# Optimization experiments

Measured on AMD Instinct MI355X. Metric: run time of the kernel, lower is better.

Reference implementation:

```python
import jax, jax.numpy as jnp
import numpy as np

B, S, E, H = 8, 2048, 512, 8
D = E // H  # head_dim = 64


def setup_inputs() -> dict:
    key0 = jax.random.key(0)
    ks = jax.random.split(key0, 12)
    scale = 1.0 / np.sqrt(E)
    return {
        "value": jax.random.normal(ks[0], (B, S, E), jnp.float32),
        "key": jax.random.normal(ks[1], (B, S, E), jnp.float32),
        "query": jax.random.normal(ks[2], (B, S, E), jnp.float32),
        "mask": jax.random.randint(ks[3], (B, 1, 1, S), 0, 2, jnp.int32),
        "wq": jax.random.normal(ks[4], (E, E), jnp.float32) * scale,
        "bq": jnp.zeros((E,), jnp.float32),
        "wk": jax.random.normal(ks[5], (E, E), jnp.float32) * scale,
        "bk": jnp.zeros((E,), jnp.float32),
        "wv": jax.random.normal(ks[6], (E, E), jnp.float32) * scale,
        "bv": jnp.zeros((E,), jnp.float32),
        "wo": jax.random.normal(ks[7], (E, E), jnp.float32) * scale,
        "bo": jnp.zeros((E,), jnp.float32),
    }


def reference(value, key, query, mask, wq, bq, wk, bk, wv, bv, wo, bo):
    b, s, e = query.shape
    # projections
    q = (query @ wq + bq).reshape(b, s, H, D)  # (B,S,H,D)
    k = (key @ wk + bk).reshape(b, s, H, D)
    v = (value @ wv + bv).reshape(b, s, H, D)
    # scaled dot-product logits: (B,H,Sq,Sk)
    logits = jnp.einsum("bqhd,bkhd->bhqk", q, k) / jnp.sqrt(jnp.asarray(D, q.dtype))
    logits = logits + mask.astype(logits.dtype) * -1e9  # mask==1 -> blocked
    attn = jax.nn.softmax(logits, axis=-1)
    out = jnp.einsum("bhqk,bkhd->bqhd", attn, v).reshape(b, s, e)
    return out @ wo + bo
```

## Files before the change

kernel.cpp:

```cpp
#include <hip/hip_runtime.h>

#define Bz 8
#define Sz 2048
#define Ez 512
#define Hz 8
#define Dz 64

typedef _Float16 f16;
typedef __attribute__((ext_vector_type(2))) _Float16 f16x2;
typedef __attribute__((ext_vector_type(8))) _Float16 f16x8;
typedef __attribute__((ext_vector_type(4))) float f32x4;

#define LOG2E 1.44269504f

__device__ __forceinline__ void async16(const void* g, void* l) {
    __builtin_amdgcn_global_load_lds(
        (const __attribute__((address_space(1))) unsigned int*)g,
        (__attribute__((address_space(3))) unsigned int*)l, 16, 0, 0);
}

__device__ __forceinline__ f16x2 pkrtz(float a, float b) {
    return __builtin_bit_cast(f16x2, __builtin_amdgcn_cvt_pkrtz(a, b));
}

__device__ __forceinline__ int swz(int row) {
    return (row & 7) ^ ((2 * ((row >> 3) & 3)) & 7);
}

__global__ __launch_bounds__(256)
void cast_kernel(const float* __restrict__ q, const float* __restrict__ k,
                 const float* __restrict__ v, const int* __restrict__ mask,
                 f16* __restrict__ qa, f16* __restrict__ ka, f16* __restrict__ va,
                 int* __restrict__ idx, int* __restrict__ slen)
{
    const int z = blockIdx.y;
    const int tid = threadIdx.x;
    if (z == 3) {
        const int b = blockIdx.x;
        if (b >= Bz) return;
        __shared__ int sc2[2][256];
        __shared__ int stot;
        const int* mp = mask + (size_t)b * Sz;
        int m[8], c = 0;
        #pragma unroll
        for (int j = 0; j < 8; ++j) { m[j] = mp[tid*8 + j]; c += (m[j] == 0); }
        sc2[0][tid] = c;
        __syncthreads();
        int src = 0;
        #pragma unroll
        for (int s = 1; s < 256; s <<= 1) {
            int vv = sc2[src][tid] + ((tid >= s) ? sc2[src][tid - s] : 0);
            sc2[src ^ 1][tid] = vv;
            src ^= 1;
            __syncthreads();
        }
        int incl = sc2[src][tid];
        int base = incl - c;
        if (tid == 255) { slen[b] = incl; stot = incl; }
        int kk = base;
        #pragma unroll
        for (int j = 0; j < 8; ++j)
            if (m[j] == 0) idx[(size_t)b * Sz + (kk++)] = tid*8 + j;
        __syncthreads();
        for (int j = stot + tid; j < Sz; j += 256) idx[(size_t)b * Sz + j] = 0;
        return;
    }
    const int i = blockIdx.x * 256 + tid;
    const float* src = (z == 0) ? q : (z == 1) ? k : v;
    f16* dst = (z == 0) ? qa : (z == 1) ? ka : va;
    float4 x = *(const float4*)&src[(size_t)i * 4];
    f16x2 h0 = pkrtz(x.x, x.y), h1 = pkrtz(x.z, x.w);
    f16 h[4] = {h0[0], h0[1], h1[0], h1[1]};
    *(uint2*)&dst[(size_t)i * 4] = *(uint2*)h;
}

__global__ __launch_bounds__(256)
void prep_w(const float* __restrict__ W0, const float* __restrict__ W1,
            const float* __restrict__ W2, const float* __restrict__ W3,
            f16* __restrict__ T0, f16* __restrict__ T1,
            f16* __restrict__ T2, f16* __restrict__ T3)
{
    __shared__ float S[64][68];
    const float* W = (blockIdx.z==0)?W0:(blockIdx.z==1)?W1:(blockIdx.z==2)?W2:W3;
    f16*         T = (blockIdx.z==0)?T0:(blockIdx.z==1)?T1:(blockIdx.z==2)?T2:T3;
    const float sc = (blockIdx.z == 0) ? 0.125f * LOG2E : 1.0f;
    const int k0 = blockIdx.x * 64, n0 = blockIdx.y * 64;
    const int tid = threadIdx.x;
    {
        int kr = tid >> 4, nc = (tid & 15) * 4;
        #pragma unroll
        for (int i = 0; i < 4; ++i) {
            float4 w4 = *(const float4*)&W[(size_t)(k0 + kr + i*16) * Ez + n0 + nc];
            S[kr + i*16][nc+0] = w4.x; S[kr + i*16][nc+1] = w4.y;
            S[kr + i*16][nc+2] = w4.z; S[kr + i*16][nc+3] = w4.w;
        }
    }
    __syncthreads();
    {
        int n = tid >> 2, kq = tid & 3;
        f16 h[16];
        #pragma unroll
        for (int j = 0; j < 16; ++j) h[j] = (f16)(S[kq*16 + j][n] * sc);
        f16* dst = &T[(size_t)(n0 + n) * Ez + k0 + kq*16];
        *(uint4*)&dst[0] = *(uint4*)&h[0];
        *(uint4*)&dst[8] = *(uint4*)&h[8];
    }
}

__global__ __launch_bounds__(256)
void compact_v(const f16* __restrict__ vp, const int* __restrict__ idx,
               const int* __restrict__ slen, f16* __restrict__ vt)
{
    const int ct = blockIdx.x, h = blockIdx.y, b = blockIdx.z;
    const int sl = slen[b];
    if (ct * 64 >= sl && !(ct == 0 && sl == 0)) return;
    __shared__ f16 S[64 * 72];
    const int tid = threadIdx.x;
    {
        int r = tid >> 2, ch = tid & 3;
        int j = ct * 64 + r;
        uint4 v0 = {0,0,0,0}, v1 = {0,0,0,0};
        if (j < sl) {
            int s = idx[(size_t)b * Sz + j];
            const f16* srcp = vp + (((size_t)b * Hz + h) * Sz + s) * Dz + ch * 16;
            v0 = *(const uint4*)&srcp[0];
            v1 = *(const uint4*)&srcp[8];
        }
        *(uint4*)&S[r*72 + ch*16]     = v0;
        *(uint4*)&S[r*72 + ch*16 + 8] = v1;
    }
    __syncthreads();
    {
        int d = tid >> 2, kq = tid & 3;
        f16 hh[16];
        #pragma unroll
        for (int j = 0; j < 16; ++j) hh[j] = S[(kq*16 + j)*72 + d];
        f16* dst = vt + (((size_t)b * Hz + h) * Dz + d) * Sz + ct*64 + kq*16;
        *(uint4*)&dst[0] = *(uint4*)&hh[0];
        *(uint4*)&dst[8] = *(uint4*)&hh[8];
    }
}

__global__ __launch_bounds__(256, 4)
void proj_gemm(const f16* __restrict__ qa, const f16* __restrict__ ka,
               const f16* __restrict__ va,
               const f16* __restrict__ wtq, const f16* __restrict__ wtk,
               const f16* __restrict__ wtv,
               const float* __restrict__ bqp, const float* __restrict__ bkp,
               const float* __restrict__ bvp,
               f16* __restrict__ qp, f16* __restrict__ kp, f16* __restrict__ vp)
{
    __shared__ __align__(16) char lds[32768];
    const int z = blockIdx.z;
    const f16* A  = (z==0)?qa:(z==1)?ka:va;
    const f16* Wt = (z==0)?wtq:(z==1)?wtk:wtv;
    const float* bias = (z==0)?bqp:(z==1)?bkp:bvp;
    f16* C16 = (z==0)?qp:(z==1)?kp:vp;
    const float bscale = (z==0) ? 0.125f*LOG2E : 1.0f;

    const int tid  = threadIdx.x;
    const int lane = tid & 63, w = tid >> 6;
    const int col  = lane & 15, quad = lane >> 4;
    const int wm = w & 1, wn = w >> 1;
    const int m0 = blockIdx.x * 128, n0 = blockIdx.y * 128;
    const int srow = lane >> 2, schunk = lane & 3;

    f32x4 acc[4][4];
    #pragma unroll
    for (int i = 0; i < 4; ++i)
        #pragma unroll
        for (int j = 0; j < 4; ++j) acc[i][j] = (f32x4){0.f,0.f,0.f,0.f};

    auto issue = [&](int t, int buf) {
        f16* As = (f16*)(lds + buf * 16384);
        f16* Ws = As + 4096;
        #pragma unroll
        for (int i = 0; i < 2; ++i) {
            int row = w*32 + i*16 + srow;
            int cl = schunk ^ ((row >> 1) & 3);
            async16(&A[(size_t)(m0 + row) * Ez + t*32 + cl*8],  &As[row*32 + schunk*8]);
            async16(&Wt[(size_t)(n0 + row) * Ez + t*32 + cl*8], &Ws[row*32 + schunk*8]);
        }
    };

    issue(0, 0);
    const int xrc = (col >> 1) & 3;

    for (int t = 0; t < 16; ++t) {
        const int cur = t & 1;
        __syncthreads();
        if (t < 15) issue(t + 1, cur ^ 1);
        f16* As = (f16*)(lds + cur * 16384);
        f16* Ws = As + 4096;
        f16x8 af[4];
        #pragma unroll
        for (int mi = 0; mi < 4; ++mi)
            af[mi] = *(const f16x8*)&As[(wm*64 + mi*16 + col)*32 + ((quad ^ xrc)*8)];
        #pragma unroll
        for (int ni = 0; ni < 4; ++ni) {
            f16x8 wf = *(const f16x8*)&Ws[(wn*64 + ni*16 + col)*32 + ((quad ^ xrc)*8)];
            #pragma unroll
            for (int mi = 0; mi < 4; ++mi)
                acc[mi][ni] = __builtin_amdgcn_mfma_f32_16x16x32_f16(af[mi], wf, acc[mi][ni], 0,0,0);
        }
    }

    f16* Tr = (f16*)lds;
    #pragma unroll
    for (int p = 0; p < 2; ++p) {
        __syncthreads();
        if (wn == p) {
            #pragma unroll
            for (int ni = 0; ni < 4; ++ni) {
                float bv = bias[n0 + p*64 + ni*16 + col] * bscale;
                #pragma unroll
                for (int mi = 0; mi < 4; ++mi)
                    #pragma unroll
                    for (int rr = 0; rr < 4; ++rr) {
                        int ml = wm*64 + mi*16 + quad*4 + rr;
                        Tr[ml*72 + ni*16 + col] = (f16)(acc[mi][ni][rr] + bv);
                    }
            }
        }
        __syncthreads();
        int rw = tid >> 1, half = tid & 1;
        int m = m0 + rw, b = m >> 11, s = m & (Sz-1);
        int hh = (n0 >> 6) + p;
        f16* dst = &C16[(((size_t)b*Hz + hh)*Sz + s)*Dz + half*32];
        const f16* srcp = &Tr[rw*72 + half*32];
        #pragma unroll
        for (int j = 0; j < 4; ++j)
            *(uint4*)&dst[j*8] = *(const uint4*)&srcp[j*8];
    }
}

__global__ __launch_bounds__(256, 4)
void out_gemm(const f16* __restrict__ A, const f16* __restrict__ Wt,
              const float* __restrict__ bias, float* __restrict__ Cf)
{
    __shared__ __align__(16) char lds[32768];
    const int tid  = threadIdx.x;
    const int lane = tid & 63, w = tid >> 6;
    const int col  = lane & 15, quad = lane >> 4;
    const int wm = w & 1, wn = w >> 1;
    const int m0 = blockIdx.x * 128, n0 = blockIdx.y * 128;
    const int srow = lane >> 2, schunk = lane & 3;

    f32x4 acc[4][4];
    #pragma unroll
    for (int i = 0; i < 4; ++i)
        #pragma unroll
        for (int j = 0; j < 4; ++j) acc[i][j] = (f32x4){0.f,0.f,0.f,0.f};

    auto issue = [&](int t, int buf) {
        f16* As = (f16*)(lds + buf * 16384);
        f16* Ws = As + 4096;
        #pragma unroll
        for (int i = 0; i < 2; ++i) {
            int row = w*32 + i*16 + srow;
            int cl = schunk ^ ((row >> 1) & 3);
            async16(&A[(size_t)(m0 + row) * Ez + t*32 + cl*8],  &As[row*32 + schunk*8]);
            async16(&Wt[(size_t)(n0 + row) * Ez + t*32 + cl*8], &Ws[row*32 + schunk*8]);
        }
    };

    issue(0, 0);
    const int xrc = (col >> 1) & 3;

    for (int t = 0; t < 16; ++t) {
        const int cur = t & 1;
        __syncthreads();
        if (t < 15) issue(t + 1, cur ^ 1);
        f16* As = (f16*)(lds + cur * 16384);
        f16* Ws = As + 4096;
        f16x8 af[4];
        #pragma unroll
        for (int mi = 0; mi < 4; ++mi)
            af[mi] = *(const f16x8*)&As[(wm*64 + mi*16 + col)*32 + ((quad ^ xrc)*8)];
        #pragma unroll
        for (int ni = 0; ni < 4; ++ni) {
            f16x8 wf = *(const f16x8*)&Ws[(wn*64 + ni*16 + col)*32 + ((quad ^ xrc)*8)];
            #pragma unroll
            for (int mi = 0; mi < 4; ++mi)
                acc[mi][ni] = __builtin_amdgcn_mfma_f32_16x16x32_f16(af[mi], wf, acc[mi][ni], 0,0,0);
        }
    }

    #pragma unroll
    for (int ni = 0; ni < 4; ++ni) {
        int n = n0 + wn*64 + ni*16 + col;
        float bv = bias[n];
        #pragma unroll
        for (int mi = 0; mi < 4; ++mi)
            #pragma unroll
            for (int rr = 0; rr < 4; ++rr) {
                int m = m0 + wm*64 + mi*16 + quad*4 + rr;
                Cf[(size_t)m * Ez + n] = acc[mi][ni][rr] + bv;
            }
    }
}

__global__ __launch_bounds__(256, 4)
void attn_f16(const f16* __restrict__ Q, const f16* __restrict__ K,
              const f16* __restrict__ VT, const int* __restrict__ idx,
              const int* __restrict__ slen, f16* __restrict__ O)
{
    __shared__ __align__(16) f16 KS[2][64*64];
    __shared__ __align__(16) f16 VS[2][64*64];

    const int tid  = threadIdx.x;
    const int lane = tid & 63, w = tid >> 6;
    const int col  = lane & 15, quad = lane >> 4;

    const int blk = blockIdx.x;
    const int xcd = blk & 7, slot = blk >> 3;
    const int bh = xcd + 8 * (slot >> 4);
    const int qb = slot & 15;
    const int b = bh >> 3, h = bh & 7;

    const int sl = slen[b];
    int nt = (sl + 63) >> 6;
    if (nt < 1) nt = 1;

    const int q0 = qb * 128 + w * 32;

    f16x8 qf[2][2];
    #pragma unroll
    for (int qt = 0; qt < 2; ++qt)
        #pragma unroll
        for (int ks = 0; ks < 2; ++ks)
            qf[qt][ks] = *(const f16x8*)&Q[((size_t)bh*Sz + q0 + qt*16 + col)*Dz + ks*32 + quad*8];

    const f16* Kp = K + (size_t)bh * Sz * Dz;
    const f16* Vp = VT + (size_t)bh * Dz * Sz;
    const int* ixp = idx + (size_t)b * Sz;

    const int srow = lane >> 3, sch = lane & 7;
    const int row0 = w*16 + srow, row1 = row0 + 8;
    const int cl0 = sch ^ swz(row0), cl1 = sch ^ swz(row1);

    int keyrow[4], gk[4];
    #pragma unroll
    for (int kc = 0; kc < 4; ++kc) {
        keyrow[kc] = 32*(kc>>1) + 8*(col>>2) + 4*(kc&1) + (col&3);
        gk[kc] = swz(keyrow[kc]);
    }

    f32x4 oacc[2][4];
    #pragma unroll
    for (int qt = 0; qt < 2; ++qt)
        #pragma unroll
        for (int dc = 0; dc < 4; ++dc) oacc[qt][dc] = (f32x4){0.f,0.f,0.f,0.f};
    const f32x4 zero4 = (f32x4){0.f, 0.f, 0.f, 0.f};
    f32x4 lacc[2] = {(f32x4){0.f,0.f,0.f,0.f}, (f32x4){0.f,0.f,0.f,0.f}};
    f16x8 one8;
    #pragma unroll
    for (int i = 0; i < 8; ++i) one8[i] = (f16)1.0f;

    auto issue = [&](int t, int buf, int s0, int s1) {
        async16(&Kp[(size_t)s0*Dz + cl0*8],          &KS[buf][row0*64 + sch*8]);
        async16(&Vp[(size_t)row0*Sz + t*64 + cl0*8], &VS[buf][row0*64 + sch*8]);
        async16(&Kp[(size_t)s1*Dz + cl1*8],          &KS[buf][row1*64 + sch*8]);
        async16(&Vp[(size_t)row1*Sz + t*64 + cl1*8], &VS[buf][row1*64 + sch*8]);
    };

    int cs0 = ixp[row0], cs1 = ixp[row1];
    issue(0, 0, cs0, cs1);
    int ns0 = 0, ns1 = 0;
    if (nt > 1) { ns0 = ixp[64 + row0]; ns1 = ixp[64 + row1]; }

    for (int t = 0; t < nt; ++t) {
        const int cur = t & 1;
        __syncthreads();
        if (t + 1 < nt) {
            issue(t + 1, cur ^ 1, ns0, ns1);
            if (t + 2 < nt) {
                ns0 = ixp[(t+2)*64 + row0];
                ns1 = ixp[(t+2)*64 + row1];
            }
        }

        f32x4 sc[2][4];
        __builtin_amdgcn_s_setprio(1);
        #pragma unroll
        for (int kc = 0; kc < 4; ++kc) {
            f16x8 kf0 = *(const f16x8*)&KS[cur][keyrow[kc]*64 + ((quad ^ gk[kc])*8)];
            f16x8 kf1 = *(const f16x8*)&KS[cur][keyrow[kc]*64 + (((4 + quad) ^ gk[kc])*8)];
            sc[0][kc] = __builtin_amdgcn_mfma_f32_16x16x32_f16(kf0, qf[0][0], zero4, 0,0,0);
            sc[1][kc] = __builtin_amdgcn_mfma_f32_16x16x32_f16(kf0, qf[1][0], zero4, 0,0,0);
            sc[0][kc] = __builtin_amdgcn_mfma_f32_16x16x32_f16(kf1, qf[0][1], sc[0][kc], 0,0,0);
            sc[1][kc] = __builtin_amdgcn_mfma_f32_16x16x32_f16(kf1, qf[1][1], sc[1][kc], 0,0,0);
        }
        __builtin_amdgcn_s_setprio(0);

        const bool last = (t == nt - 1);
        union { f16x2 h2[4]; f16x8 h8; } ph[2][2];
        #pragma unroll
        for (int qt = 0; qt < 2; ++qt) {
            #pragma unroll
            for (int kg = 0; kg < 2; ++kg) {
                float e0 = __builtin_amdgcn_exp2f(sc[qt][2*kg][0]);
                float e1 = __builtin_amdgcn_exp2f(sc[qt][2*kg][1]);
                float e2 = __builtin_amdgcn_exp2f(sc[qt][2*kg][2]);
                float e3 = __builtin_amdgcn_exp2f(sc[qt][2*kg][3]);
                float e4 = __builtin_amdgcn_exp2f(sc[qt][2*kg+1][0]);
                float e5 = __builtin_amdgcn_exp2f(sc[qt][2*kg+1][1]);
                float e6 = __builtin_amdgcn_exp2f(sc[qt][2*kg+1][2]);
                float e7 = __builtin_amdgcn_exp2f(sc[qt][2*kg+1][3]);
                if (last) {
                    int rem = sl - t*64 - 32*kg - 8*quad;
                    e0 = (rem > 0) ? e0 : 0.f; e1 = (rem > 1) ? e1 : 0.f;
                    e2 = (rem > 2) ? e2 : 0.f; e3 = (rem > 3) ? e3 : 0.f;
                    e4 = (rem > 4) ? e4 : 0.f; e5 = (rem > 5) ? e5 : 0.f;
                    e6 = (rem > 6) ? e6 : 0.f; e7 = (rem > 7) ? e7 : 0.f;
                }
                ph[qt][kg].h2[0] = pkrtz(e0, e1);
                ph[qt][kg].h2[1] = pkrtz(e2, e3);
                ph[qt][kg].h2[2] = pkrtz(e4, e5);
                ph[qt][kg].h2[3] = pkrtz(e6, e7);
            }
        }

        __builtin_amdgcn_s_setprio(1);
        lacc[0] = __builtin_amdgcn_mfma_f32_16x16x32_f16(one8, ph[0][0].h8, lacc[0], 0,0,0);
        lacc[1] = __builtin_amdgcn_mfma_f32_16x16x32_f16(one8, ph[1][0].h8, lacc[1], 0,0,0);
        lacc[0] = __builtin_amdgcn_mfma_f32_16x16x32_f16(one8, ph[0][1].h8, lacc[0], 0,0,0);
        lacc[1] = __builtin_amdgcn_mfma_f32_16x16x32_f16(one8, ph[1][1].h8, lacc[1], 0,0,0);
        #pragma unroll
        for (int dc = 0; dc < 4; ++dc) {
            const int d = dc*16 + col;
            const int gd = swz(d);
            #pragma unroll
            for (int kg = 0; kg < 2; ++kg) {
                f16x8 vf = *(const f16x8*)&VS[cur][d*64 + (((kg*4 + quad) ^ gd)*8)];
                oacc[0][dc] = __builtin_amdgcn_mfma_f32_16x16x32_f16(vf, ph[0][kg].h8, oacc[0][dc], 0,0,0);
                oacc[1][dc] = __builtin_amdgcn_mfma_f32_16x16x32_f16(vf, ph[1][kg].h8, oacc[1][dc], 0,0,0);
            }
        }
        __builtin_amdgcn_s_setprio(0);
    }

    float inv[2];
    inv[0] = 1.0f / lacc[0][0];
    inv[1] = 1.0f / lacc[1][0];
    #pragma unroll
    for (int qt = 0; qt < 2; ++qt) {
        const int q = q0 + qt*16 + col;
        f16* op = &O[((size_t)b*Sz + q)*Ez + h*Dz];
        #pragma unroll
        for (int dc = 0; dc < 4; ++dc) {
            f16 ov[4] = {(f16)(oacc[qt][dc][0]*inv[qt]), (f16)(oacc[qt][dc][1]*inv[qt]),
                         (f16)(oacc[qt][dc][2]*inv[qt]), (f16)(oacc[qt][dc][3]*inv[qt])};
            *(uint2*)&op[dc*16 + quad*4] = *(uint2*)ov;
        }
    }
}

extern "C" void kernel_launch(void* const* d_in, const int* in_sizes, int n_in,
                              void* d_out, int out_size, void* d_ws, size_t ws_size,
                              hipStream_t stream)
{
    const float* value = (const float*)d_in[0];
    const float* key   = (const float*)d_in[1];
    const float* query = (const float*)d_in[2];
    const int*   mask  = (const int*)d_in[3];
    const float* wq = (const float*)d_in[4];
    const float* bq = (const float*)d_in[5];
    const float* wk = (const float*)d_in[6];
    const float* bk = (const float*)d_in[7];
    const float* wv = (const float*)d_in[8];
    const float* bv = (const float*)d_in[9];
    const float* wo = (const float*)d_in[10];
    const float* bo = (const float*)d_in[11];
    float* out = (float*)d_out;

    const size_t nW   = (size_t)Ez * Ez;
    const size_t nAct = (size_t)Bz * Sz * Ez;
    f16* wtq = (f16*)d_ws;
    f16* wtk = wtq + nW;
    f16* wtv = wtk + nW;
    f16* wto = wtv + nW;
    f16* qa  = wto + nW;
    f16* ka  = qa + nAct;
    f16* va  = ka + nAct;
    f16* qp  = va + nAct;
    f16* kp  = qp + nAct;
    f16* vp  = kp + nAct;
    f16* vt  = vp + nAct;
    f16* o16 = vt + nAct;
    int* idxp = (int*)(o16 + nAct);
    int* slenp = idxp + Bz * Sz;

    cast_kernel<<<dim3(8192, 4), 256, 0, stream>>>(query, key, value, mask,
                                                   qa, ka, va, idxp, slenp);
    prep_w<<<dim3(8, 8, 4), 256, 0, stream>>>(wq, wk, wv, wo, wtq, wtk, wtv, wto);

    proj_gemm<<<dim3(128, 4, 3), 256, 0, stream>>>(qa, ka, va, wtq, wtk, wtv,
                                                   bq, bk, bv, qp, kp, vp);

    compact_v<<<dim3(32, Hz, Bz), 256, 0, stream>>>(vp, idxp, slenp, vt);

    attn_f16<<<1024, 256, 0, stream>>>(qp, kp, vt, idxp, slenp, o16);

    out_gemm<<<dim3(128, 4), 256, 0, stream>>>(o16, wto, bo, out);
}
```

Measured before the change: 281.4 us.

## Scatter K/V into compacted order in projection epilogue instead of gathering in attention

The mask prefix-scan now emits a per-position rank (or -1 for masked keys) instead of a list of gather indices. The K/V projection epilogue uses this rank to write unmasked rows directly to compacted positions and skips storing masked rows. As a result, compact_v and the attention kernel read contiguous rows, with no index lookups and no dependent index loads in the async prefetch loop. The trade-off is that rows past the compacted length in K are no longer padded with valid data, so correctness relies on the last-tile masking in attention.

```diff
diff --git a/kernel.cpp b/kernel.cpp
--- a/kernel.cpp
+++ b/kernel.cpp
@@ -31,7 +31,7 @@
 void cast_kernel(const float* __restrict__ q, const float* __restrict__ k,
                  const float* __restrict__ v, const int* __restrict__ mask,
                  f16* __restrict__ qa, f16* __restrict__ ka, f16* __restrict__ va,
-                 int* __restrict__ idx, int* __restrict__ slen)
+                 int* __restrict__ rnk, int* __restrict__ slen)
 {
     const int z = blockIdx.y;
     const int tid = threadIdx.x;
@@ -39,7 +39,6 @@
         const int b = blockIdx.x;
         if (b >= Bz) return;
         __shared__ int sc2[2][256];
-        __shared__ int stot;
         const int* mp = mask + (size_t)b * Sz;
         int m[8], c = 0;
         #pragma unroll
@@ -56,13 +55,16 @@
         }
         int incl = sc2[src][tid];
         int base = incl - c;
-        if (tid == 255) { slen[b] = incl; stot = incl; }
+        if (tid == 255) slen[b] = incl;
         int kk = base;
-        #pragma unroll
-        for (int j = 0; j < 8; ++j)
-            if (m[j] == 0) idx[(size_t)b * Sz + (kk++)] = tid*8 + j;
-        __syncthreads();
-        for (int j = stot + tid; j < Sz; j += 256) idx[(size_t)b * Sz + j] = 0;
+        int r8[8];
+        #pragma unroll
+        for (int j = 0; j < 8; ++j) {
+            r8[j] = (m[j] == 0) ? kk : -1;
+            kk += (m[j] == 0);
+        }
+        #pragma unroll
+        for (int j = 0; j < 8; ++j) rnk[(size_t)b * Sz + tid*8 + j] = r8[j];
         return;
     }
     const int i = blockIdx.x * 256 + tid;
@@ -108,8 +110,8 @@
 }
 
 __global__ __launch_bounds__(256)
-void compact_v(const f16* __restrict__ vp, const int* __restrict__ idx,
-               const int* __restrict__ slen, f16* __restrict__ vt)
+void compact_v(const f16* __restrict__ vp, const int* __restrict__ slen,
+               f16* __restrict__ vt)
 {
     const int ct = blockIdx.x, h = blockIdx.y, b = blockIdx.z;
     const int sl = slen[b];
@@ -121,8 +123,7 @@
         int j = ct * 64 + r;
         uint4 v0 = {0,0,0,0}, v1 = {0,0,0,0};
         if (j < sl) {
-            int s = idx[(size_t)b * Sz + j];
-            const f16* srcp = vp + (((size_t)b * Hz + h) * Sz + s) * Dz + ch * 16;
+            const f16* srcp = vp + (((size_t)b * Hz + h) * Sz + j) * Dz + ch * 16;
             v0 = *(const uint4*)&srcp[0];
             v1 = *(const uint4*)&srcp[8];
         }
@@ -147,7 +148,7 @@
                const f16* __restrict__ wtq, const f16* __restrict__ wtk,
                const f16* __restrict__ wtv,
                const float* __restrict__ bqp, const float* __restrict__ bkp,
-               const float* __restrict__ bvp,
+               const float* __restrict__ bvp, const int* __restrict__ rnk,
                f16* __restrict__ qp, f16* __restrict__ kp, f16* __restrict__ vp)
 {
     __shared__ __align__(16) char lds[32768];
@@ -203,6 +204,16 @@
             for (int mi = 0; mi < 4; ++mi)
                 acc[mi][ni] = __builtin_amdgcn_mfma_f32_16x16x32_f16(af[mi], wf, acc[mi][ni], 0,0,0);
         }
+    }
+
+    const int rw = tid >> 1, half = tid & 1;
+    const int m = m0 + rw, b = m >> 11, s = m & (Sz-1);
+    int rowout = s;
+    bool dostore = true;
+    if (z != 0) {
+        int rk = rnk[(size_t)b * Sz + s];
+        dostore = (rk >= 0);
+        rowout = rk;
     }
 
     f16* Tr = (f16*)lds;
@@ -223,14 +234,14 @@
             }
         }
         __syncthreads();
-        int rw = tid >> 1, half = tid & 1;
-        int m = m0 + rw, b = m >> 11, s = m & (Sz-1);
-        int hh = (n0 >> 6) + p;
-        f16* dst = &C16[(((size_t)b*Hz + hh)*Sz + s)*Dz + half*32];
-        const f16* srcp = &Tr[rw*72 + half*32];
-        #pragma unroll
-        for (int j = 0; j < 4; ++j)
-            *(uint4*)&dst[j*8] = *(const uint4*)&srcp[j*8];
+        if (dostore) {
+            int hh = (n0 >> 6) + p;
+            f16* dst = &C16[(((size_t)b*Hz + hh)*Sz + rowout)*Dz + half*32];
+            const f16* srcp = &Tr[rw*72 + half*32];
+            #pragma unroll
+            for (int j = 0; j < 4; ++j)
+                *(uint4*)&dst[j*8] = *(const uint4*)&srcp[j*8];
+        }
     }
 }
 
@@ -302,8 +313,8 @@
 
 __global__ __launch_bounds__(256, 4)
 void attn_f16(const f16* __restrict__ Q, const f16* __restrict__ K,
-              const f16* __restrict__ VT, const int* __restrict__ idx,
-              const int* __restrict__ slen, f16* __restrict__ O)
+              const f16* __restrict__ VT, const int* __restrict__ slen,
+              f16* __restrict__ O)
 {
     __shared__ __align__(16) f16 KS[2][64*64];
     __shared__ __align__(16) f16 VS[2][64*64];
@@ -333,7 +344,6 @@
 
     const f16* Kp = K + (size_t)bh * Sz * Dz;
     const f16* Vp = VT + (size_t)bh * Dz * Sz;
-    const int* ixp = idx + (size_t)b * Sz;
 
     const int srow = lane >> 3, sch = lane & 7;
     const int row0 = w*16 + srow, row1 = row0 + 8;
@@ -357,28 +367,19 @@
     #pragma unroll
     for (int i = 0; i < 8; ++i) one8[i] = (f16)1.0f;
 
-    auto issue = [&](int t, int buf, int s0, int s1) {
-        async16(&Kp[(size_t)s0*Dz + cl0*8],          &KS[buf][row0*64 + sch*8]);
-        async16(&Vp[(size_t)row0*Sz + t*64 + cl0*8], &VS[buf][row0*64 + sch*8]);
-        async16(&Kp[(size_t)s1*Dz + cl1*8],          &KS[buf][row1*64 + sch*8]);
-        async16(&Vp[(size_t)row1*Sz + t*64 + cl1*8], &VS[buf][row1*64 + sch*8]);
+    auto issue = [&](int t, int buf) {
+        async16(&Kp[(size_t)(t*64 + row0)*Dz + cl0*8], &KS[buf][row0*64 + sch*8]);
+        async16(&Vp[(size_t)row0*Sz + t*64 + cl0*8],   &VS[buf][row0*64 + sch*8]);
+        async16(&Kp[(size_t)(t*64 + row1)*Dz + cl1*8], &KS[buf][row1*64 + sch*8]);
+        async16(&Vp[(size_t)row1*Sz + t*64 + cl1*8],   &VS[buf][row1*64 + sch*8]);
     };
 
-    int cs0 = ixp[row0], cs1 = ixp[row1];
-    issue(0, 0, cs0, cs1);
-    int ns0 = 0, ns1 = 0;
-    if (nt > 1) { ns0 = ixp[64 + row0]; ns1 = ixp[64 + row1]; }
+    issue(0, 0);
 
     for (int t = 0; t < nt; ++t) {
         const int cur = t & 1;
         __syncthreads();
-        if (t + 1 < nt) {
-            issue(t + 1, cur ^ 1, ns0, ns1);
-            if (t + 2 < nt) {
-                ns0 = ixp[(t+2)*64 + row0];
-                ns1 = ixp[(t+2)*64 + row1];
-            }
-        }
+        if (t + 1 < nt) issue(t + 1, cur ^ 1);
 
         f32x4 sc[2][4];
         __builtin_amdgcn_s_setprio(1);
@@ -488,19 +489,19 @@
     f16* vp  = kp + nAct;
     f16* vt  = vp + nAct;
     f16* o16 = vt + nAct;
-    int* idxp = (int*)(o16 + nAct);
-    int* slenp = idxp + Bz * Sz;
+    int* rnkp = (int*)(o16 + nAct);
+    int* slenp = rnkp + Bz * Sz;
 
     cast_kernel<<<dim3(8192, 4), 256, 0, stream>>>(query, key, value, mask,
-                                                   qa, ka, va, idxp, slenp);
+                                                   qa, ka, va, rnkp, slenp);
     prep_w<<<dim3(8, 8, 4), 256, 0, stream>>>(wq, wk, wv, wo, wtq, wtk, wtv, wto);
 
     proj_gemm<<<dim3(128, 4, 3), 256, 0, stream>>>(qa, ka, va, wtq, wtk, wtv,
-                                                   bq, bk, bv, qp, kp, vp);
-
-    compact_v<<<dim3(32, Hz, Bz), 256, 0, stream>>>(vp, idxp, slenp, vt);
-
-    attn_f16<<<1024, 256, 0, stream>>>(qp, kp, vt, idxp, slenp, o16);
+                                                   bq, bk, bv, rnkp, qp, kp, vp);
+
+    compact_v<<<dim3(32, Hz, Bz), 256, 0, stream>>>(vp, slenp, vt);
+
+    attn_f16<<<1024, 256, 0, stream>>>(qp, kp, vt, slenp, o16);
 
     out_gemm<<<dim3(128, 4), 256, 0, stream>>>(o16, wto, bo, out);
 }
```

Result: faster. 273.3 us (-2.9%).
